# Kernel optimization log

Hardware: AMD Instinct MI355X
Metric: run time of the kernel (lower is better)

## Reference

```python
import jax, jax.numpy as jnp
import numpy as np

C_M, C_Z, H, C_HID = 256, 128, 8, 32
N_SEQ, N_RES = 64, 384
INF = 1e9
EPS = 1e-5


def layernorm(x, w, b):
    mu = jnp.mean(x, axis=-1, keepdims=True)
    var = jnp.mean(jnp.square(x - mu), axis=-1, keepdims=True)
    return (x - mu) * jax.lax.rsqrt(var + EPS) * w + b


def setup_inputs() -> dict:
    key = jax.random.key(0)
    ks = jax.random.split(key, 6)
    m = jax.random.normal(ks[0], (N_SEQ, N_RES, C_M), dtype=jnp.float32)
    z = jax.random.normal(ks[1], (N_RES, N_RES, C_Z), dtype=jnp.float32)
    mask = jnp.ones((N_SEQ, N_RES), dtype=jnp.float32)
    return {
        "m": m,
        "z": z,
        "mask": mask,
        "ln_m_w": jnp.ones((C_M,), jnp.float32),
        "ln_m_b": jnp.zeros((C_M,), jnp.float32),
        "ln_z_w": jnp.ones((C_Z,), jnp.float32),
        "ln_z_b": jnp.zeros((C_Z,), jnp.float32),
        "W_z": jax.random.normal(ks[2], (C_Z, H), jnp.float32) * 0.05,
        "W_v": jax.random.normal(ks[3], (C_M, H * C_HID), jnp.float32) * 0.05,
        "W_g": jax.random.normal(ks[4], (C_M, H * C_HID), jnp.float32) * 0.05,
        "W_o": jax.random.normal(ks[5], (H * C_HID, C_M), jnp.float32) * 0.05,
    }


def reference(m, z, mask, ln_m_w, ln_m_b, ln_z_w, ln_z_b, W_z, W_v, W_g, W_o):
    S, N = m.shape[0], m.shape[1]
    # mask: max over MSA rows, keepdim -> [1, N]; bias -> [1,1,1,N]
    mask_max = jnp.max(mask, axis=-2, keepdims=True)
    mask_bias = (INF * (mask_max - 1.0))[:, None, None, :]  # [1,1,1,N]
    # pair bias: LN(z) @ W_z -> [N,N,H] -> [H,N,N]
    zb = layernorm(z, ln_z_w, ln_z_b) @ W_z  # [N,N,H]
    zb = jnp.transpose(zb, (2, 0, 1))  # [H,N,N]
    # LN on m
    m_ln = layernorm(m, ln_m_w, ln_m_b)  # [S,N,C_m]
    # values: [S,N,H*c] -> [S,H,N,c]
    v = (m_ln @ W_v).reshape(S, N, H, C_HID).transpose(0, 2, 1, 3)
    # attention weights from summed biases (no QK): [1,H,N,N] after broadcast
    a = jax.nn.softmax(mask_bias + zb[None], axis=-1)  # [1,H,N,N]
    # o = a @ v  -> [S,H,N,c]
    o = jnp.einsum('hqk,shkc->shqc', a[0], v)
    o = o.transpose(0, 2, 1, 3)  # [S,N,H,c]
    # sigmoid gate
    g = jax.nn.sigmoid(m_ln @ W_g).reshape(S, N, H, C_HID)
    o = (o * g).reshape(S, N, H * C_HID)
    return o @ W_o  # [S,N,C_m]
```

## Files before the change

### kernel.cpp

```cpp
#include <hip/hip_runtime.h>
#include <math.h>

#define S 64
#define NRES 384
#define CM 256
#define CZ 128
#define NH 8
#define CH 32
#define HC 256
#define NROW 147456

typedef unsigned short u16;
typedef __attribute__((ext_vector_type(8))) short bf16x8;
typedef __attribute__((ext_vector_type(4))) float f32x4;
typedef __attribute__((ext_vector_type(8))) unsigned short ushort8;
typedef __attribute__((ext_vector_type(4))) unsigned short ushort4_t;

#define OFF_BIAS 0
#define OFF_WT   200704
#define OFF_WOT  462848
#define OFF_A    593920
#define OFF_VT   2953216
#define OFF_G    15536128
#define OFF_O    28119040
#define OFF_MLN  40701952
#define OFF_ZB   OFF_O

__device__ __forceinline__ u16 f2bf(float f) {
    union { float f; unsigned int u; } v; v.f = f;
    unsigned int u = v.u;
    u += 0x7fff + ((u >> 16) & 1);
    return (u16)(u >> 16);
}
__device__ __forceinline__ float bf2f(u16 b) {
    union { float f; unsigned int u; } v; v.u = ((unsigned int)b) << 16;
    return v.f;
}
__device__ __forceinline__ void gload16(const u16* g, u16* l) {
    __builtin_amdgcn_global_load_lds(
        (const __attribute__((address_space(1))) void*)g,
        (__attribute__((address_space(3))) void*)l, 16, 0, 0);
}

__global__ __launch_bounds__(256) void k_stage1(
        const float* __restrict__ z, const float* __restrict__ Wz,
        const float* __restrict__ lzw, const float* __restrict__ lzb,
        const float* __restrict__ mask,
        const float* __restrict__ Wv, const float* __restrict__ Wg,
        const float* __restrict__ Wo, const float* __restrict__ m,
        const float* __restrict__ lmw, const float* __restrict__ lmb,
        float* __restrict__ zb, float* __restrict__ bias,
        u16* __restrict__ Wt, u16* __restrict__ Wot, u16* __restrict__ mln) {
    const int bid = blockIdx.x, tid = threadIdx.x;
    if (bid < 1152) {
        __shared__ u16 sWWT[16 * 128];
        __shared__ float sPart[2][2][8];
        const int wave = tid >> 6, lane = tid & 63;
        const int rl = lane & 15, kg = lane >> 4;
        if (tid < 128) {
            const int c = tid;
            const float4 wz0 = *(const float4*)&Wz[c * 8];
            const float4 wz1 = *(const float4*)&Wz[c * 8 + 4];
            const float lw = lzw[c], lbv = lzb[c];
            float wzv[8] = {wz0.x, wz0.y, wz0.z, wz0.w, wz1.x, wz1.y, wz1.z, wz1.w};
            float ww[8], wb[8];
            #pragma unroll
            for (int h = 0; h < 8; ++h) {
                ww[h] = lw * wzv[h];
                wb[h] = lbv * wzv[h];
                sWWT[h * 128 + c] = f2bf(ww[h]);
                sWWT[(8 + h) * 128 + c] = 0;
            }
            #pragma unroll
            for (int h = 0; h < 8; ++h) {
                #pragma unroll
                for (int off = 1; off < 64; off <<= 1) {
                    ww[h] += __shfl_xor(ww[h], off);
                    wb[h] += __shfl_xor(wb[h], off);
                }
            }
            if (lane == 0) {
                #pragma unroll
                for (int h = 0; h < 8; ++h) {
                    sPart[wave][0][h] = ww[h];
                    sPart[wave][1][h] = wb[h];
                }
            }
        }
        __syncthreads();
        const float c1 = (rl < 8) ? (sPart[0][0][rl] + sPart[1][0][rl]) : 0.f;
        const float c2 = (rl < 8) ? (sPart[0][1][rl] + sPart[1][1][rl]) : 0.f;
        bf16x8 bfr[4];
        #pragma unroll
        for (int t = 0; t < 4; ++t)
            bfr[t] = *(const bf16x8*)&sWWT[rl * 128 + kg * 8 + t * 32];
        #pragma unroll
        for (int it = 0; it < 2; ++it) {
            const int row0 = bid * 128 + it * 64 + wave * 16;
            const float* zrow = z + (size_t)(row0 + rl) * CZ + kg * 8;
            bf16x8 af[4];
            float sm = 0.f, sq = 0.f;
            #pragma unroll
            for (int t = 0; t < 4; ++t) {
                const float4 x0 = *(const float4*)&zrow[t * 32];
                const float4 x1 = *(const float4*)&zrow[t * 32 + 4];
                float xs[8] = {x0.x, x0.y, x0.z, x0.w, x1.x, x1.y, x1.z, x1.w};
                u16 tmp[8];
                #pragma unroll
                for (int e = 0; e < 8; ++e) {
                    sm += xs[e]; sq += xs[e] * xs[e];
                    tmp[e] = f2bf(xs[e]);
                }
                af[t] = *(bf16x8*)tmp;
            }
            sm += __shfl_xor(sm, 16); sq += __shfl_xor(sq, 16);
            sm += __shfl_xor(sm, 32); sq += __shfl_xor(sq, 32);
            const float mu = sm * (1.0f / CZ);
            const float var = sq * (1.0f / CZ) - mu * mu;
            const float rs = rsqrtf(var + 1e-5f);
            f32x4 acc = {};
            #pragma unroll
            for (int t = 0; t < 4; ++t)
                acc = __builtin_amdgcn_mfma_f32_16x16x32_bf16(af[t], bfr[t], acc, 0, 0, 0);
            f32x4 pv;
            #pragma unroll
            for (int r = 0; r < 4; ++r) {
                const int rr = kg * 4 + r;
                const float mu_r = __shfl(mu, rr);
                const float rs_r = __shfl(rs, rr);
                pv[r] = rs_r * (acc[r] - mu_r * c1) + c2;
            }
            if (rl < 8)
                *(f32x4*)&zb[(size_t)rl * NROW + row0 + kg * 4] = pv;
        }
    } else if (bid < 1154) {
        const int k = (bid - 1152) * 256 + tid;
        if (k < NRES) {
            float mx = -1e30f;
            for (int s = 0; s < S; ++s) mx = fmaxf(mx, mask[s * NRES + k]);
            bias[k] = 1e9f * (mx - 1.0f);
        }
    } else if (bid < 1666) {
        const int i = (bid - 1154) * 256 + tid;
        const int n = i >> 8, k = i & 255;
        const float v = (n < HC) ? Wv[(size_t)k * HC + n] : Wg[(size_t)k * HC + (n - HC)];
        Wt[i] = f2bf(v);
    } else if (bid < 1922) {
        const int i = (bid - 1666) * 256 + tid;
        const int n = i >> 8, k = i & 255;
        Wot[i] = f2bf(Wo[(size_t)k * CM + n]);
    } else {
        const int row = (bid - 1922) * 4 + (tid >> 6);
        const int lane = tid & 63;
        const float4 x = *(const float4*)&m[(size_t)row * CM + lane * 4];
        float sm = x.x + x.y + x.z + x.w;
        float sq = x.x*x.x + x.y*x.y + x.z*x.z + x.w*x.w;
        #pragma unroll
        for (int off = 32; off >= 1; off >>= 1) {
            sm += __shfl_xor(sm, off);
            sq += __shfl_xor(sq, off);
        }
        const float mu = sm * (1.0f / CM);
        const float var = sq * (1.0f / CM) - mu * mu;
        const float rs = rsqrtf(var + 1e-5f);
        const float4 w4 = *(const float4*)&lmw[lane * 4];
        const float4 b4 = *(const float4*)&lmb[lane * 4];
        u16 t4[4];
        t4[0] = f2bf((x.x - mu) * rs * w4.x + b4.x);
        t4[1] = f2bf((x.y - mu) * rs * w4.y + b4.y);
        t4[2] = f2bf((x.z - mu) * rs * w4.z + b4.z);
        t4[3] = f2bf((x.w - mu) * rs * w4.w + b4.w);
        *(ushort4_t*)&mln[(size_t)row * CM + lane * 4] = *(ushort4_t*)t4;
    }
}

__global__ __launch_bounds__(256) void k_stage2(
        const u16* __restrict__ mln, const u16* __restrict__ Wt,
        const float* __restrict__ zb, const float* __restrict__ bias,
        u16* __restrict__ vt, u16* __restrict__ g_, u16* __restrict__ a_out) {
    __shared__ u16 As[128][32];
    __shared__ u16 Bs[128][32];
    const int bid = blockIdx.x, tid = threadIdx.x;
    if (bid >= 768) {
        const int w = (bid - 768) * 4 + (tid >> 6);
        const int lane = tid & 63;
        const int h = w & 7, q = w >> 3;
        const float* zbh = zb + (size_t)h * NROW + (size_t)q * NRES;
        float v[6];
        float mx = -1e30f;
        #pragma unroll
        for (int t = 0; t < 6; ++t) {
            const int k = lane + 64 * t;
            v[t] = zbh[k] + bias[k];
            mx = fmaxf(mx, v[t]);
        }
        #pragma unroll
        for (int off = 32; off >= 1; off >>= 1) mx = fmaxf(mx, __shfl_xor(mx, off));
        float sum = 0.f;
        #pragma unroll
        for (int t = 0; t < 6; ++t) { v[t] = expf(v[t] - mx); sum += v[t]; }
        #pragma unroll
        for (int off = 32; off >= 1; off >>= 1) sum += __shfl_xor(sum, off);
        const float inv = 1.0f / sum;
        #pragma unroll
        for (int t = 0; t < 6; ++t)
            a_out[((size_t)h * NRES + q) * NRES + lane + 64 * t] = f2bf(v[t] * inv);
        return;
    }
    const int xcd = bid & 7, idx = bid >> 3;
    const int nt = idx & 3, mt = xcd * 24 + (idx >> 2);
    const int m0 = mt * 128, n0 = nt * 128;
    const int wave = tid >> 6, lane = tid & 63;
    const int wm = (wave >> 1) * 64, wn = (wave & 1) * 64;
    const int rl = lane & 15, kg = lane >> 4;
    const int lr = lane >> 2, lk = (lane & 3) * 8;
    const int wr = wave * 32;
    const u16* ag  = mln + (size_t)(m0 + wr + lr) * CM + lk;
    const u16* ag2 = ag + 16 * CM;
    const u16* bg  = Wt + (size_t)(n0 + wr + lr) * CM + lk;
    const u16* bg2 = bg + 16 * CM;
    u16* al  = &As[wr][0];
    u16* al2 = &As[wr + 16][0];
    u16* bl  = &Bs[wr][0];
    u16* bl2 = &Bs[wr + 16][0];
    const bool vhalf = (n0 < HC);
    f32x4 acc[4][4] = {};
    for (int kt = 0; kt < CM; kt += 32) {
        if (kt) __syncthreads();
        gload16(ag + kt, al);  gload16(ag2 + kt, al2);
        gload16(bg + kt, bl);  gload16(bg2 + kt, bl2);
        __syncthreads();
        bf16x8 af[4], bfr[4];
        #pragma unroll
        for (int i = 0; i < 4; ++i) af[i]  = *(const bf16x8*)&As[wm + i*16 + rl][kg*8];
        #pragma unroll
        for (int j = 0; j < 4; ++j) bfr[j] = *(const bf16x8*)&Bs[wn + j*16 + rl][kg*8];
        if (vhalf) {
            #pragma unroll
            for (int j = 0; j < 4; ++j)
                #pragma unroll
                for (int i = 0; i < 4; ++i)
                    acc[j][i] = __builtin_amdgcn_mfma_f32_16x16x32_bf16(bfr[j], af[i], acc[j][i], 0, 0, 0);
        } else {
            #pragma unroll
            for (int i = 0; i < 4; ++i)
                #pragma unroll
                for (int j = 0; j < 4; ++j)
                    acc[i][j] = __builtin_amdgcn_mfma_f32_16x16x32_bf16(af[i], bfr[j], acc[i][j], 0, 0, 0);
        }
    }
    if (vhalf) {
        #pragma unroll
        for (int j = 0; j < 4; ++j)
            #pragma unroll
            for (int r = 0; r < 4; ++r) {
                const int vcol = n0 + wn + j*16 + kg*4 + r;
                const int h = vcol >> 5, c = vcol & 31;
                #pragma unroll
                for (int i = 0; i < 4; ++i) {
                    const int mrowb = m0 + wm + i*16;
                    const int s = mrowb / NRES;
                    const int nn = mrowb - s * NRES + rl;
                    vt[(((size_t)h * S + s) * CH + c) * NRES + nn] = f2bf(acc[j][i][r]);
                }
            }
    } else {
        #pragma unroll
        for (int i = 0; i < 4; ++i)
            #pragma unroll
            for (int r = 0; r < 4; ++r) {
                const int row = m0 + wm + i*16 + kg*4 + r;
                #pragma unroll
                for (int j = 0; j < 4; ++j) {
                    const int gc = n0 + wn + j*16 + rl - HC;
                    g_[(size_t)row * HC + gc] = f2bf(1.0f / (1.0f + expf(-acc[i][j][r])));
                }
            }
    }
}

__global__ __launch_bounds__(256) void k_attn2(const u16* __restrict__ a_,
        const u16* __restrict__ vt, u16* __restrict__ o_) {
    __shared__ u16 As[128][32];
    __shared__ u16 Bs[128][32];
    const int tid = threadIdx.x;
    const int h = blockIdx.x & 7, rem = blockIdx.x >> 3;
    const int mt = rem >> 4, nt = rem & 15;
    const int q0 = mt * 128, sc0 = nt * 128;
    const int wave = tid >> 6, lane = tid & 63;
    const int wm = (wave >> 1) * 64, wn = (wave & 1) * 64;
    const int rl = lane & 15, kg = lane >> 4;
    const int lr = lane >> 2, lk = (lane & 3) * 8;
    const int wr = wave * 32;
    const u16* ag  = a_ + (size_t)h * NRES * NRES + (size_t)(q0 + wr + lr) * NRES + lk;
    const u16* ag2 = ag + 16 * NRES;
    const u16* bg  = vt + (size_t)h * S * CH * NRES + (size_t)(sc0 + wr + lr) * NRES + lk;
    const u16* bg2 = bg + 16 * NRES;
    u16* al  = &As[wr][0];
    u16* al2 = &As[wr + 16][0];
    u16* bl  = &Bs[wr][0];
    u16* bl2 = &Bs[wr + 16][0];
    f32x4 acc[4][4] = {};
    for (int kt = 0; kt < NRES; kt += 32) {
        if (kt) __syncthreads();
        gload16(ag + kt, al);  gload16(ag2 + kt, al2);
        gload16(bg + kt, bl);  gload16(bg2 + kt, bl2);
        __syncthreads();
        bf16x8 af[4], bfr[4];
        #pragma unroll
        for (int i = 0; i < 4; ++i) af[i]  = *(const bf16x8*)&As[wm + i*16 + rl][kg*8];
        #pragma unroll
        for (int j = 0; j < 4; ++j) bfr[j] = *(const bf16x8*)&Bs[wn + j*16 + rl][kg*8];
        #pragma unroll
        for (int i = 0; i < 4; ++i)
            #pragma unroll
            for (int j = 0; j < 4; ++j)
                acc[i][j] = __builtin_amdgcn_mfma_f32_16x16x32_bf16(af[i], bfr[j], acc[i][j], 0, 0, 0);
    }
    #pragma unroll
    for (int i = 0; i < 4; ++i)
        #pragma unroll
        for (int r = 0; r < 4; ++r) {
            const int q = q0 + wm + i*16 + kg*4 + r;
            #pragma unroll
            for (int j = 0; j < 4; ++j) {
                const int sc = sc0 + wn + j*16 + rl;
                const int s = sc >> 5, c = sc & 31;
                o_[(((size_t)s * NRES + q) * NH + h) * CH + c] = f2bf(acc[i][j][r]);
            }
        }
}

__global__ __launch_bounds__(256) void k_gemm_out(const u16* __restrict__ o_,
        const u16* __restrict__ g_, const u16* __restrict__ Wot,
        float* __restrict__ out) {
    __shared__ u16 As[128][40];
    __shared__ u16 Bs[128][32];
    const int tid = threadIdx.x;
    const int xcd = blockIdx.x & 7, idx = blockIdx.x >> 3;
    const int nt = idx & 1, mt = xcd * 24 + (idx >> 1);
    const int m0 = mt * 128, n0 = nt * 128;
    const int wave = tid >> 6, lane = tid & 63;
    const int wm = (wave >> 1) * 64, wn = (wave & 1) * 64;
    const int rl = lane & 15, kg = lane >> 4;
    const int lr = lane >> 2, lk = (lane & 3) * 8;
    const int wr = wave * 32;
    const int sr = tid >> 1, sh = (tid & 1) * 16;
    const u16* orow = o_ + (size_t)(m0 + sr) * HC;
    const u16* grow = g_ + (size_t)(m0 + sr) * HC;
    const u16* bg  = Wot + (size_t)(n0 + wr + lr) * HC + lk;
    const u16* bg2 = bg + 16 * HC;
    u16* bl  = &Bs[wr][0];
    u16* bl2 = &Bs[wr + 16][0];
    f32x4 acc[4][4] = {};
    for (int kt = 0; kt < HC; kt += 32) {
        if (kt) __syncthreads();
        gload16(bg + kt, bl);  gload16(bg2 + kt, bl2);
        {
            u16 tmp[16];
            const ushort8 ov0 = *(const ushort8*)&orow[kt + sh];
            const ushort8 ov1 = *(const ushort8*)&orow[kt + sh + 8];
            const ushort8 gv0 = *(const ushort8*)&grow[kt + sh];
            const ushort8 gv1 = *(const ushort8*)&grow[kt + sh + 8];
            #pragma unroll
            for (int p = 0; p < 8; ++p) {
                tmp[p]     = f2bf(bf2f(ov0[p]) * bf2f(gv0[p]));
                tmp[p + 8] = f2bf(bf2f(ov1[p]) * bf2f(gv1[p]));
            }
            *(ushort8*)&As[sr][sh]     = *(ushort8*)&tmp[0];
            *(ushort8*)&As[sr][sh + 8] = *(ushort8*)&tmp[8];
        }
        __syncthreads();
        bf16x8 af[4], bfr[4];
        #pragma unroll
        for (int i = 0; i < 4; ++i) af[i]  = *(const bf16x8*)&As[wm + i*16 + rl][kg*8];
        #pragma unroll
        for (int j = 0; j < 4; ++j) bfr[j] = *(const bf16x8*)&Bs[wn + j*16 + rl][kg*8];
        #pragma unroll
        for (int i = 0; i < 4; ++i)
            #pragma unroll
            for (int j = 0; j < 4; ++j)
                acc[i][j] = __builtin_amdgcn_mfma_f32_16x16x32_bf16(af[i], bfr[j], acc[i][j], 0, 0, 0);
    }
    #pragma unroll
    for (int i = 0; i < 4; ++i)
        #pragma unroll
        for (int r = 0; r < 4; ++r) {
            const int row = m0 + wm + i*16 + kg*4 + r;
            #pragma unroll
            for (int j = 0; j < 4; ++j)
                out[(size_t)row * CM + n0 + wn + j*16 + rl] = acc[i][j][r];
        }
}

extern "C" void kernel_launch(void* const* d_in, const int* in_sizes, int n_in,
                              void* d_out, int out_size, void* d_ws, size_t ws_size,
                              hipStream_t stream) {
    const float* m      = (const float*)d_in[0];
    const float* z      = (const float*)d_in[1];
    const float* mask   = (const float*)d_in[2];
    const float* ln_m_w = (const float*)d_in[3];
    const float* ln_m_b = (const float*)d_in[4];
    const float* ln_z_w = (const float*)d_in[5];
    const float* ln_z_b = (const float*)d_in[6];
    const float* Wz     = (const float*)d_in[7];
    const float* Wv     = (const float*)d_in[8];
    const float* Wg     = (const float*)d_in[9];
    const float* Wo     = (const float*)d_in[10];
    float* out = (float*)d_out;
    char* ws = (char*)d_ws;

    float* bias = (float*)(ws + OFF_BIAS);
    u16* Wt     = (u16*)(ws + OFF_WT);
    u16* Wot    = (u16*)(ws + OFF_WOT);
    u16* a      = (u16*)(ws + OFF_A);
    u16* vtw    = (u16*)(ws + OFF_VT);
    u16* gw     = (u16*)(ws + OFF_G);
    u16* ow     = (u16*)(ws + OFF_O);
    u16* mlnw   = (u16*)(ws + OFF_MLN);
    float* zbw  = (float*)(ws + OFF_ZB);

    k_stage1<<<8066, 256, 0, stream>>>(z, Wz, ln_z_w, ln_z_b, mask, Wv, Wg, Wo,
                                       m, ln_m_w, ln_m_b, zbw, bias, Wt, Wot, mlnw);
    k_stage2<<<1536, 256, 0, stream>>>(mlnw, Wt, zbw, bias, vtw, gw, a);
    k_attn2<<<384, 256, 0, stream>>>(a, vtw, ow);
    k_gemm_out<<<384, 256, 0, stream>>>(ow, gw, Wot, out);
}
```

Before: 76.77 us.

## Fuse pair-bias LayerNorm projection with softmax per query row in shared memory

Moves the LN(z)@W_z computation out of stage1 and into the softmax blocks of the main kernel. Each of 384 blocks now handles one query row: it stages z through shared memory, computes all 8 head logits with MFMA into LDS, then runs the softmax directly. This removes the fp32 zb round-trip through global memory and one dependency boundary. In exchange, z is processed by only 384 blocks using about 50KB of shared memory each, which may lower occupancy and parallelism for the z-read phase.

```diff
diff --git a/kernel.cpp b/kernel.cpp
--- a/kernel.cpp
+++ b/kernel.cpp
@@ -24,7 +24,6 @@
 #define OFF_G    15536128
 #define OFF_O    28119040
 #define OFF_MLN  40701952
-#define OFF_ZB   OFF_O
 
 __device__ __forceinline__ u16 f2bf(float f) {
     union { float f; unsigned int u; } v; v.f = f;
@@ -42,115 +41,32 @@
         (__attribute__((address_space(3))) void*)l, 16, 0, 0);
 }
 
-__global__ __launch_bounds__(256) void k_stage1(
-        const float* __restrict__ z, const float* __restrict__ Wz,
-        const float* __restrict__ lzw, const float* __restrict__ lzb,
+__global__ __launch_bounds__(256) void k_misc(
         const float* __restrict__ mask,
         const float* __restrict__ Wv, const float* __restrict__ Wg,
         const float* __restrict__ Wo, const float* __restrict__ m,
         const float* __restrict__ lmw, const float* __restrict__ lmb,
-        float* __restrict__ zb, float* __restrict__ bias,
-        u16* __restrict__ Wt, u16* __restrict__ Wot, u16* __restrict__ mln) {
+        float* __restrict__ bias, u16* __restrict__ Wt, u16* __restrict__ Wot,
+        u16* __restrict__ mln) {
     const int bid = blockIdx.x, tid = threadIdx.x;
-    if (bid < 1152) {
-        __shared__ u16 sWWT[16 * 128];
-        __shared__ float sPart[2][2][8];
-        const int wave = tid >> 6, lane = tid & 63;
-        const int rl = lane & 15, kg = lane >> 4;
-        if (tid < 128) {
-            const int c = tid;
-            const float4 wz0 = *(const float4*)&Wz[c * 8];
-            const float4 wz1 = *(const float4*)&Wz[c * 8 + 4];
-            const float lw = lzw[c], lbv = lzb[c];
-            float wzv[8] = {wz0.x, wz0.y, wz0.z, wz0.w, wz1.x, wz1.y, wz1.z, wz1.w};
-            float ww[8], wb[8];
-            #pragma unroll
-            for (int h = 0; h < 8; ++h) {
-                ww[h] = lw * wzv[h];
-                wb[h] = lbv * wzv[h];
-                sWWT[h * 128 + c] = f2bf(ww[h]);
-                sWWT[(8 + h) * 128 + c] = 0;
-            }
-            #pragma unroll
-            for (int h = 0; h < 8; ++h) {
-                #pragma unroll
-                for (int off = 1; off < 64; off <<= 1) {
-                    ww[h] += __shfl_xor(ww[h], off);
-                    wb[h] += __shfl_xor(wb[h], off);
-                }
-            }
-            if (lane == 0) {
-                #pragma unroll
-                for (int h = 0; h < 8; ++h) {
-                    sPart[wave][0][h] = ww[h];
-                    sPart[wave][1][h] = wb[h];
-                }
-            }
-        }
-        __syncthreads();
-        const float c1 = (rl < 8) ? (sPart[0][0][rl] + sPart[1][0][rl]) : 0.f;
-        const float c2 = (rl < 8) ? (sPart[0][1][rl] + sPart[1][1][rl]) : 0.f;
-        bf16x8 bfr[4];
-        #pragma unroll
-        for (int t = 0; t < 4; ++t)
-            bfr[t] = *(const bf16x8*)&sWWT[rl * 128 + kg * 8 + t * 32];
-        #pragma unroll
-        for (int it = 0; it < 2; ++it) {
-            const int row0 = bid * 128 + it * 64 + wave * 16;
-            const float* zrow = z + (size_t)(row0 + rl) * CZ + kg * 8;
-            bf16x8 af[4];
-            float sm = 0.f, sq = 0.f;
-            #pragma unroll
-            for (int t = 0; t < 4; ++t) {
-                const float4 x0 = *(const float4*)&zrow[t * 32];
-                const float4 x1 = *(const float4*)&zrow[t * 32 + 4];
-                float xs[8] = {x0.x, x0.y, x0.z, x0.w, x1.x, x1.y, x1.z, x1.w};
-                u16 tmp[8];
-                #pragma unroll
-                for (int e = 0; e < 8; ++e) {
-                    sm += xs[e]; sq += xs[e] * xs[e];
-                    tmp[e] = f2bf(xs[e]);
-                }
-                af[t] = *(bf16x8*)tmp;
-            }
-            sm += __shfl_xor(sm, 16); sq += __shfl_xor(sq, 16);
-            sm += __shfl_xor(sm, 32); sq += __shfl_xor(sq, 32);
-            const float mu = sm * (1.0f / CZ);
-            const float var = sq * (1.0f / CZ) - mu * mu;
-            const float rs = rsqrtf(var + 1e-5f);
-            f32x4 acc = {};
-            #pragma unroll
-            for (int t = 0; t < 4; ++t)
-                acc = __builtin_amdgcn_mfma_f32_16x16x32_bf16(af[t], bfr[t], acc, 0, 0, 0);
-            f32x4 pv;
-            #pragma unroll
-            for (int r = 0; r < 4; ++r) {
-                const int rr = kg * 4 + r;
-                const float mu_r = __shfl(mu, rr);
-                const float rs_r = __shfl(rs, rr);
-                pv[r] = rs_r * (acc[r] - mu_r * c1) + c2;
-            }
-            if (rl < 8)
-                *(f32x4*)&zb[(size_t)rl * NROW + row0 + kg * 4] = pv;
-        }
-    } else if (bid < 1154) {
-        const int k = (bid - 1152) * 256 + tid;
+    if (bid < 2) {
+        const int k = bid * 256 + tid;
         if (k < NRES) {
             float mx = -1e30f;
             for (int s = 0; s < S; ++s) mx = fmaxf(mx, mask[s * NRES + k]);
             bias[k] = 1e9f * (mx - 1.0f);
         }
-    } else if (bid < 1666) {
-        const int i = (bid - 1154) * 256 + tid;
+    } else if (bid < 514) {
+        const int i = (bid - 2) * 256 + tid;
         const int n = i >> 8, k = i & 255;
         const float v = (n < HC) ? Wv[(size_t)k * HC + n] : Wg[(size_t)k * HC + (n - HC)];
         Wt[i] = f2bf(v);
-    } else if (bid < 1922) {
-        const int i = (bid - 1666) * 256 + tid;
+    } else if (bid < 770) {
+        const int i = (bid - 514) * 256 + tid;
         const int n = i >> 8, k = i & 255;
         Wot[i] = f2bf(Wo[(size_t)k * CM + n]);
     } else {
-        const int row = (bid - 1922) * 4 + (tid >> 6);
+        const int row = (bid - 770) * 4 + (tid >> 6);
         const int lane = tid & 63;
         const float4 x = *(const float4*)&m[(size_t)row * CM + lane * 4];
         float sm = x.x + x.y + x.z + x.w;
@@ -174,55 +90,151 @@
     }
 }
 
-__global__ __launch_bounds__(256) void k_stage2(
+__global__ __launch_bounds__(256) void k_main(
+        const float* __restrict__ z, const float* __restrict__ Wz,
+        const float* __restrict__ lzw, const float* __restrict__ lzb,
+        const float* __restrict__ bias,
         const u16* __restrict__ mln, const u16* __restrict__ Wt,
-        const float* __restrict__ zb, const float* __restrict__ bias,
-        u16* __restrict__ vt, u16* __restrict__ g_, u16* __restrict__ a_out) {
-    __shared__ u16 As[128][32];
-    __shared__ u16 Bs[128][32];
+        u16* __restrict__ a_out, u16* __restrict__ vt, u16* __restrict__ g_) {
+    __shared__ float smem[12544];
     const int bid = blockIdx.x, tid = threadIdx.x;
-    if (bid >= 768) {
-        const int w = (bid - 768) * 4 + (tid >> 6);
-        const int lane = tid & 63;
-        const int h = w & 7, q = w >> 3;
-        const float* zbh = zb + (size_t)h * NROW + (size_t)q * NRES;
-        float v[6];
-        float mx = -1e30f;
-        #pragma unroll
-        for (int t = 0; t < 6; ++t) {
-            const int k = lane + 64 * t;
-            v[t] = zbh[k] + bias[k];
-            mx = fmaxf(mx, v[t]);
-        }
-        #pragma unroll
-        for (int off = 32; off >= 1; off >>= 1) mx = fmaxf(mx, __shfl_xor(mx, off));
-        float sum = 0.f;
-        #pragma unroll
-        for (int t = 0; t < 6; ++t) { v[t] = expf(v[t] - mx); sum += v[t]; }
-        #pragma unroll
-        for (int off = 32; off >= 1; off >>= 1) sum += __shfl_xor(sum, off);
-        const float inv = 1.0f / sum;
-        #pragma unroll
-        for (int t = 0; t < 6; ++t)
-            a_out[((size_t)h * NRES + q) * NRES + lane + 64 * t] = f2bf(v[t] * inv);
+    const int wave = tid >> 6, lane = tid & 63;
+    const int rl = lane & 15, kg = lane >> 4;
+
+    if (bid < 384) {
+        const int q = bid;
+        float* sZ   = smem;
+        float* sLg  = smem + 8320;
+        u16*  sW    = (u16*)(smem + 11456);
+        float* sPart = smem + 12480;
+
+        if (tid < 128) {
+            const int c = tid;
+            const float4 wz0 = *(const float4*)&Wz[c * 8];
+            const float4 wz1 = *(const float4*)&Wz[c * 8 + 4];
+            const float lw = lzw[c], lbv = lzb[c];
+            float wzv[8] = {wz0.x, wz0.y, wz0.z, wz0.w, wz1.x, wz1.y, wz1.z, wz1.w};
+            float ww[8], wb[8];
+            #pragma unroll
+            for (int h = 0; h < 8; ++h) {
+                ww[h] = lw * wzv[h];
+                wb[h] = lbv * wzv[h];
+                sW[h * 128 + c] = f2bf(ww[h]);
+                sW[(8 + h) * 128 + c] = 0;
+            }
+            #pragma unroll
+            for (int h = 0; h < 8; ++h) {
+                #pragma unroll
+                for (int off = 1; off < 64; off <<= 1) {
+                    ww[h] += __shfl_xor(ww[h], off);
+                    wb[h] += __shfl_xor(wb[h], off);
+                }
+            }
+            if (lane == 0) {
+                #pragma unroll
+                for (int h = 0; h < 8; ++h) {
+                    sPart[wave * 16 + h]     = ww[h];
+                    sPart[wave * 16 + 8 + h] = wb[h];
+                }
+            }
+        }
+        __syncthreads();
+        const float c1 = (rl < 8) ? (sPart[rl] + sPart[16 + rl]) : 0.f;
+        const float c2 = (rl < 8) ? (sPart[8 + rl] + sPart[24 + rl]) : 0.f;
+        bf16x8 bfr[4];
+        #pragma unroll
+        for (int t = 0; t < 4; ++t)
+            bfr[t] = *(const bf16x8*)&sW[rl * 128 + kg * 8 + t * 32];
+
+        float* sZw = sZ + wave * 2080;
+        const float4* zq = (const float4*)(z + (size_t)q * NRES * CZ);
+        for (int c = 0; c < 6; ++c) {
+            const float4* src = zq + (size_t)(c * 64 + wave * 16) * (CZ / 4);
+            #pragma unroll
+            for (int p = 0; p < 8; ++p) {
+                const int fi = p * 64 + lane;
+                const int r = fi >> 5, c4 = fi & 31;
+                *(float4*)&sZw[r * 130 + c4 * 4] = src[fi];
+            }
+            float sm = 0.f, sq = 0.f;
+            bf16x8 af[4];
+            #pragma unroll
+            for (int t = 0; t < 4; ++t) {
+                const f32x4 x0 = *(const f32x4*)&sZw[rl * 130 + t * 32 + kg * 8];
+                const f32x4 x1 = *(const f32x4*)&sZw[rl * 130 + t * 32 + kg * 8 + 4];
+                float xs[8] = {x0[0], x0[1], x0[2], x0[3], x1[0], x1[1], x1[2], x1[3]};
+                u16 tmp[8];
+                #pragma unroll
+                for (int e = 0; e < 8; ++e) {
+                    sm += xs[e]; sq += xs[e] * xs[e];
+                    tmp[e] = f2bf(xs[e]);
+                }
+                af[t] = *(bf16x8*)tmp;
+            }
+            sm += __shfl_xor(sm, 16); sq += __shfl_xor(sq, 16);
+            sm += __shfl_xor(sm, 32); sq += __shfl_xor(sq, 32);
+            const float mu = sm * (1.0f / CZ);
+            const float var = sq * (1.0f / CZ) - mu * mu;
+            const float rs = rsqrtf(var + 1e-5f);
+            f32x4 acc = {};
+            #pragma unroll
+            for (int t = 0; t < 4; ++t)
+                acc = __builtin_amdgcn_mfma_f32_16x16x32_bf16(af[t], bfr[t], acc, 0, 0, 0);
+            f32x4 pv;
+            #pragma unroll
+            for (int r = 0; r < 4; ++r) {
+                const int rr = kg * 4 + r;
+                const float mu_r = __shfl(mu, rr);
+                const float rs_r = __shfl(rs, rr);
+                pv[r] = rs_r * (acc[r] - mu_r * c1) + c2;
+            }
+            if (rl < 8)
+                *(f32x4*)&sLg[rl * 392 + c * 64 + wave * 16 + kg * 4] = pv;
+        }
+        __syncthreads();
+        #pragma unroll
+        for (int hh = 0; hh < 2; ++hh) {
+            const int h = wave + hh * 4;
+            float v[6];
+            float mx = -1e30f;
+            #pragma unroll
+            for (int t = 0; t < 6; ++t) {
+                const int k = lane + 64 * t;
+                v[t] = sLg[h * 392 + k] + bias[k];
+                mx = fmaxf(mx, v[t]);
+            }
+            #pragma unroll
+            for (int off = 32; off >= 1; off >>= 1) mx = fmaxf(mx, __shfl_xor(mx, off));
+            float sum = 0.f;
+            #pragma unroll
+            for (int t = 0; t < 6; ++t) { v[t] = expf(v[t] - mx); sum += v[t]; }
+            #pragma unroll
+            for (int off = 32; off >= 1; off >>= 1) sum += __shfl_xor(sum, off);
+            const float inv = 1.0f / sum;
+            #pragma unroll
+            for (int t = 0; t < 6; ++t)
+                a_out[((size_t)h * NRES + q) * NRES + lane + 64 * t] = f2bf(v[t] * inv);
+        }
         return;
     }
-    const int xcd = bid & 7, idx = bid >> 3;
+
+    const int bb = bid - 384;
+    const int xcd = bb & 7, idx = bb >> 3;
     const int nt = idx & 3, mt = xcd * 24 + (idx >> 2);
     const int m0 = mt * 128, n0 = nt * 128;
-    const int wave = tid >> 6, lane = tid & 63;
     const int wm = (wave >> 1) * 64, wn = (wave & 1) * 64;
-    const int rl = lane & 15, kg = lane >> 4;
     const int lr = lane >> 2, lk = (lane & 3) * 8;
     const int wr = wave * 32;
+    u16* As = (u16*)smem;
+    u16* Bs = As + 128 * 32;
     const u16* ag  = mln + (size_t)(m0 + wr + lr) * CM + lk;
     const u16* ag2 = ag + 16 * CM;
     const u16* bg  = Wt + (size_t)(n0 + wr + lr) * CM + lk;
     const u16* bg2 = bg + 16 * CM;
-    u16* al  = &As[wr][0];
-    u16* al2 = &As[wr + 16][0];
-    u16* bl  = &Bs[wr][0];
-    u16* bl2 = &Bs[wr + 16][0];
+    u16* al  = As + wr * 32;
+    u16* al2 = As + (wr + 16) * 32;
+    u16* bl  = Bs + wr * 32;
+    u16* bl2 = Bs + (wr + 16) * 32;
     const bool vhalf = (n0 < HC);
     f32x4 acc[4][4] = {};
     for (int kt = 0; kt < CM; kt += 32) {
@@ -232,9 +244,9 @@
         __syncthreads();
         bf16x8 af[4], bfr[4];
         #pragma unroll
-        for (int i = 0; i < 4; ++i) af[i]  = *(const bf16x8*)&As[wm + i*16 + rl][kg*8];
-        #pragma unroll
-        for (int j = 0; j < 4; ++j) bfr[j] = *(const bf16x8*)&Bs[wn + j*16 + rl][kg*8];
+        for (int i = 0; i < 4; ++i) af[i]  = *(const bf16x8*)&As[(wm + i*16 + rl) * 32 + kg*8];
+        #pragma unroll
+        for (int j = 0; j < 4; ++j) bfr[j] = *(const bf16x8*)&Bs[(wn + j*16 + rl) * 32 + kg*8];
         if (vhalf) {
             #pragma unroll
             for (int j = 0; j < 4; ++j)
@@ -418,11 +430,11 @@
     u16* gw     = (u16*)(ws + OFF_G);
     u16* ow     = (u16*)(ws + OFF_O);
     u16* mlnw   = (u16*)(ws + OFF_MLN);
-    float* zbw  = (float*)(ws + OFF_ZB);
-
-    k_stage1<<<8066, 256, 0, stream>>>(z, Wz, ln_z_w, ln_z_b, mask, Wv, Wg, Wo,
-                                       m, ln_m_w, ln_m_b, zbw, bias, Wt, Wot, mlnw);
-    k_stage2<<<1536, 256, 0, stream>>>(mlnw, Wt, zbw, bias, vtw, gw, a);
+
+    k_misc<<<6914, 256, 0, stream>>>(mask, Wv, Wg, Wo, m, ln_m_w, ln_m_b,
+                                     bias, Wt, Wot, mlnw);
+    k_main<<<1152, 256, 0, stream>>>(z, Wz, ln_z_w, ln_z_b, bias, mlnw, Wt,
+                                     a, vtw, gw);
     k_attn2<<<384, 256, 0, stream>>>(a, vtw, ow);
     k_gemm_out<<<384, 256, 0, stream>>>(ow, gw, Wot, out);
 }
```

After: 97.04 us. 1.26x slower.

## Stage z rows through LDS with coalesced loads and halve rows per block

Applied to the files above, without the earlier changes.

The z layernorm+projection part of stage1 now loads each block's 64 rows of z into padded shared memory using fully coalesced float4 loads, then reads fragments from LDS instead of strided global loads. Blocks process 64 rows instead of 128, doubling the block count for that branch, and grid offsets for the other branches are shifted to match. This targets poor global coalescing of the per-lane strided z reads. In exchange it adds about 37KB of static shared memory to every block of the fused kernel, including branches that never use it, which may reduce occupancy.

```diff
diff --git a/kernel.cpp b/kernel.cpp
--- a/kernel.cpp
+++ b/kernel.cpp
@@ -51,12 +51,15 @@
         const float* __restrict__ lmw, const float* __restrict__ lmb,
         float* __restrict__ zb, float* __restrict__ bias,
         u16* __restrict__ Wt, u16* __restrict__ Wot, u16* __restrict__ mln) {
+    __shared__ float smem[9376];
     const int bid = blockIdx.x, tid = threadIdx.x;
-    if (bid < 1152) {
-        __shared__ u16 sWWT[16 * 128];
-        __shared__ float sPart[2][2][8];
+    if (bid < 2304) {
+        float* sZ   = smem;
+        u16*  sW    = (u16*)(smem + 8320);
+        float* sPart = smem + 9344;
         const int wave = tid >> 6, lane = tid & 63;
         const int rl = lane & 15, kg = lane >> 4;
+        const int row0 = bid * 64;
         if (tid < 128) {
             const int c = tid;
             const float4 wz0 = *(const float4*)&Wz[c * 8];
@@ -68,8 +71,8 @@
             for (int h = 0; h < 8; ++h) {
                 ww[h] = lw * wzv[h];
                 wb[h] = lbv * wzv[h];
-                sWWT[h * 128 + c] = f2bf(ww[h]);
-                sWWT[(8 + h) * 128 + c] = 0;
+                sW[h * 128 + c] = f2bf(ww[h]);
+                sW[(8 + h) * 128 + c] = 0;
             }
             #pragma unroll
             for (int h = 0; h < 8; ++h) {
@@ -82,75 +85,78 @@
             if (lane == 0) {
                 #pragma unroll
                 for (int h = 0; h < 8; ++h) {
-                    sPart[wave][0][h] = ww[h];
-                    sPart[wave][1][h] = wb[h];
+                    sPart[wave * 16 + h]     = ww[h];
+                    sPart[wave * 16 + 8 + h] = wb[h];
                 }
             }
         }
+        const float4* zq = (const float4*)(z + (size_t)row0 * CZ);
+        #pragma unroll
+        for (int i = 0; i < 8; ++i) {
+            const int fi = tid + i * 256;
+            const int r = fi >> 5, c4 = fi & 31;
+            *(float4*)&sZ[r * 130 + c4 * 4] = zq[fi];
+        }
         __syncthreads();
-        const float c1 = (rl < 8) ? (sPart[0][0][rl] + sPart[1][0][rl]) : 0.f;
-        const float c2 = (rl < 8) ? (sPart[0][1][rl] + sPart[1][1][rl]) : 0.f;
+        const float c1 = (rl < 8) ? (sPart[rl] + sPart[16 + rl]) : 0.f;
+        const float c2 = (rl < 8) ? (sPart[8 + rl] + sPart[24 + rl]) : 0.f;
         bf16x8 bfr[4];
         #pragma unroll
         for (int t = 0; t < 4; ++t)
-            bfr[t] = *(const bf16x8*)&sWWT[rl * 128 + kg * 8 + t * 32];
-        #pragma unroll
-        for (int it = 0; it < 2; ++it) {
-            const int row0 = bid * 128 + it * 64 + wave * 16;
-            const float* zrow = z + (size_t)(row0 + rl) * CZ + kg * 8;
-            bf16x8 af[4];
-            float sm = 0.f, sq = 0.f;
-            #pragma unroll
-            for (int t = 0; t < 4; ++t) {
-                const float4 x0 = *(const float4*)&zrow[t * 32];
-                const float4 x1 = *(const float4*)&zrow[t * 32 + 4];
-                float xs[8] = {x0.x, x0.y, x0.z, x0.w, x1.x, x1.y, x1.z, x1.w};
-                u16 tmp[8];
-                #pragma unroll
-                for (int e = 0; e < 8; ++e) {
-                    sm += xs[e]; sq += xs[e] * xs[e];
-                    tmp[e] = f2bf(xs[e]);
-                }
-                af[t] = *(bf16x8*)tmp;
-            }
-            sm += __shfl_xor(sm, 16); sq += __shfl_xor(sq, 16);
-            sm += __shfl_xor(sm, 32); sq += __shfl_xor(sq, 32);
-            const float mu = sm * (1.0f / CZ);
-            const float var = sq * (1.0f / CZ) - mu * mu;
-            const float rs = rsqrtf(var + 1e-5f);
-            f32x4 acc = {};
-            #pragma unroll
-            for (int t = 0; t < 4; ++t)
-                acc = __builtin_amdgcn_mfma_f32_16x16x32_bf16(af[t], bfr[t], acc, 0, 0, 0);
-            f32x4 pv;
-            #pragma unroll
-            for (int r = 0; r < 4; ++r) {
-                const int rr = kg * 4 + r;
-                const float mu_r = __shfl(mu, rr);
-                const float rs_r = __shfl(rs, rr);
-                pv[r] = rs_r * (acc[r] - mu_r * c1) + c2;
-            }
-            if (rl < 8)
-                *(f32x4*)&zb[(size_t)rl * NROW + row0 + kg * 4] = pv;
-        }
-    } else if (bid < 1154) {
-        const int k = (bid - 1152) * 256 + tid;
+            bfr[t] = *(const bf16x8*)&sW[rl * 128 + kg * 8 + t * 32];
+        const float* zrow = sZ + (wave * 16 + rl) * 130 + kg * 8;
+        bf16x8 af[4];
+        float sm = 0.f, sq = 0.f;
+        #pragma unroll
+        for (int t = 0; t < 4; ++t) {
+            const f32x4 x0 = *(const f32x4*)&zrow[t * 32];
+            const f32x4 x1 = *(const f32x4*)&zrow[t * 32 + 4];
+            float xs[8] = {x0[0], x0[1], x0[2], x0[3], x1[0], x1[1], x1[2], x1[3]};
+            u16 tmp[8];
+            #pragma unroll
+            for (int e = 0; e < 8; ++e) {
+                sm += xs[e]; sq += xs[e] * xs[e];
+                tmp[e] = f2bf(xs[e]);
+            }
+            af[t] = *(bf16x8*)tmp;
+        }
+        sm += __shfl_xor(sm, 16); sq += __shfl_xor(sq, 16);
+        sm += __shfl_xor(sm, 32); sq += __shfl_xor(sq, 32);
+        const float mu = sm * (1.0f / CZ);
+        const float var = sq * (1.0f / CZ) - mu * mu;
+        const float rs = rsqrtf(var + 1e-5f);
+        f32x4 acc = {};
+        #pragma unroll
+        for (int t = 0; t < 4; ++t)
+            acc = __builtin_amdgcn_mfma_f32_16x16x32_bf16(af[t], bfr[t], acc, 0, 0, 0);
+        f32x4 pv;
+        #pragma unroll
+        for (int r = 0; r < 4; ++r) {
+            const int rr = kg * 4 + r;
+            const float mu_r = __shfl(mu, rr);
+            const float rs_r = __shfl(rs, rr);
+            pv[r] = rs_r * (acc[r] - mu_r * c1) + c2;
+        }
+        if (rl < 8)
+            *(f32x4*)&zb[(size_t)rl * NROW + row0 + wave * 16 + kg * 4] = pv;
+    } else if (bid < 2306) {
+        const int k = (bid - 2304) * 256 + tid;
         if (k < NRES) {
             float mx = -1e30f;
             for (int s = 0; s < S; ++s) mx = fmaxf(mx, mask[s * NRES + k]);
             bias[k] = 1e9f * (mx - 1.0f);
         }
-    } else if (bid < 1666) {
-        const int i = (bid - 1154) * 256 + tid;
+    } else if (bid < 2818) {
+        const int i = (bid - 2306) * 256 + tid;
         const int n = i >> 8, k = i & 255;
         const float v = (n < HC) ? Wv[(size_t)k * HC + n] : Wg[(size_t)k * HC + (n - HC)];
         Wt[i] = f2bf(v);
-    } else if (bid < 1922) {
-        const int i = (bid - 1666) * 256 + tid;
+    } else if (bid < 3074) {
+        const int i = (bid - 2818) * 256 + tid;
         const int n = i >> 8, k = i & 255;
         Wot[i] = f2bf(Wo[(size_t)k * CM + n]);
     } else {
-        const int row = (bid - 1922) * 4 + (tid >> 6);
+        const int row = (bid - 3074) * 4 + (tid >> 6);
         const int lane = tid & 63;
         const float4 x = *(const float4*)&m[(size_t)row * CM + lane * 4];
         float sm = x.x + x.y + x.z + x.w;
@@ -420,7 +426,7 @@
     u16* mlnw   = (u16*)(ws + OFF_MLN);
     float* zbw  = (float*)(ws + OFF_ZB);
 
-    k_stage1<<<8066, 256, 0, stream>>>(z, Wz, ln_z_w, ln_z_b, mask, Wv, Wg, Wo,
+    k_stage1<<<9218, 256, 0, stream>>>(z, Wz, ln_z_w, ln_z_b, mask, Wv, Wg, Wo,
                                        m, ln_m_w, ln_m_b, zbw, bias, Wt, Wot, mlnw);
     k_stage2<<<1536, 256, 0, stream>>>(mlnw, Wt, zbw, bias, vtw, gw, a);
     k_attn2<<<384, 256, 0, stream>>>(a, vtw, ow);
```

Result: slower. 83.60 us (+8.9%).

## Split pair-bias LN+projection into dedicated kernel with coalesced LDS-staged z loads

Applied to the files above, without the earlier changes.

Moves the folded LayerNorm weight and bias sums (WWT, C1, C2) into a small precompute block of a separate misc kernel, so they are no longer recomputed in every pair-bias block. A new k_zb kernel reads z fully coalesced, converts it to bf16 and stages it through swizzled LDS before the MFMA projection. Each block now loops over 4 row groups. This targets the strided z loads and the redundant per-block weight prep. In exchange it adds an extra kernel launch and a global round trip for the weights.

```diff
diff --git a/kernel.cpp b/kernel.cpp
--- a/kernel.cpp
+++ b/kernel.cpp
@@ -17,6 +17,9 @@
 typedef __attribute__((ext_vector_type(4))) unsigned short ushort4_t;
 
 #define OFF_BIAS 0
+#define OFF_WWT  8192
+#define OFF_C1   16384
+#define OFF_C2   16448
 #define OFF_WT   200704
 #define OFF_WOT  462848
 #define OFF_A    593920
@@ -42,21 +45,26 @@
         (__attribute__((address_space(3))) void*)l, 16, 0, 0);
 }
 
-__global__ __launch_bounds__(256) void k_stage1(
-        const float* __restrict__ z, const float* __restrict__ Wz,
+__global__ __launch_bounds__(256) void k_misc(
+        const float* __restrict__ mask, const float* __restrict__ Wz,
         const float* __restrict__ lzw, const float* __restrict__ lzb,
-        const float* __restrict__ mask,
         const float* __restrict__ Wv, const float* __restrict__ Wg,
         const float* __restrict__ Wo, const float* __restrict__ m,
         const float* __restrict__ lmw, const float* __restrict__ lmb,
-        float* __restrict__ zb, float* __restrict__ bias,
+        float* __restrict__ bias, u16* __restrict__ WWT,
+        float* __restrict__ C1, float* __restrict__ C2,
         u16* __restrict__ Wt, u16* __restrict__ Wot, u16* __restrict__ mln) {
+    __shared__ float sP[2][2][8];
     const int bid = blockIdx.x, tid = threadIdx.x;
-    if (bid < 1152) {
-        __shared__ u16 sWWT[16 * 128];
-        __shared__ float sPart[2][2][8];
+    if (bid < 2) {
+        const int k = bid * 256 + tid;
+        if (k < NRES) {
+            float mx = -1e30f;
+            for (int s = 0; s < S; ++s) mx = fmaxf(mx, mask[s * NRES + k]);
+            bias[k] = 1e9f * (mx - 1.0f);
+        }
+    } else if (bid == 2) {
         const int wave = tid >> 6, lane = tid & 63;
-        const int rl = lane & 15, kg = lane >> 4;
         if (tid < 128) {
             const int c = tid;
             const float4 wz0 = *(const float4*)&Wz[c * 8];
@@ -68,8 +76,8 @@
             for (int h = 0; h < 8; ++h) {
                 ww[h] = lw * wzv[h];
                 wb[h] = lbv * wzv[h];
-                sWWT[h * 128 + c] = f2bf(ww[h]);
-                sWWT[(8 + h) * 128 + c] = 0;
+                WWT[h * 128 + c] = f2bf(ww[h]);
+                WWT[(8 + h) * 128 + c] = 0;
             }
             #pragma unroll
             for (int h = 0; h < 8; ++h) {
@@ -82,75 +90,27 @@
             if (lane == 0) {
                 #pragma unroll
                 for (int h = 0; h < 8; ++h) {
-                    sPart[wave][0][h] = ww[h];
-                    sPart[wave][1][h] = wb[h];
+                    sP[wave][0][h] = ww[h];
+                    sP[wave][1][h] = wb[h];
                 }
             }
         }
         __syncthreads();
-        const float c1 = (rl < 8) ? (sPart[0][0][rl] + sPart[1][0][rl]) : 0.f;
-        const float c2 = (rl < 8) ? (sPart[0][1][rl] + sPart[1][1][rl]) : 0.f;
-        bf16x8 bfr[4];
-        #pragma unroll
-        for (int t = 0; t < 4; ++t)
-            bfr[t] = *(const bf16x8*)&sWWT[rl * 128 + kg * 8 + t * 32];
-        #pragma unroll
-        for (int it = 0; it < 2; ++it) {
-            const int row0 = bid * 128 + it * 64 + wave * 16;
-            const float* zrow = z + (size_t)(row0 + rl) * CZ + kg * 8;
-            bf16x8 af[4];
-            float sm = 0.f, sq = 0.f;
-            #pragma unroll
-            for (int t = 0; t < 4; ++t) {
-                const float4 x0 = *(const float4*)&zrow[t * 32];
-                const float4 x1 = *(const float4*)&zrow[t * 32 + 4];
-                float xs[8] = {x0.x, x0.y, x0.z, x0.w, x1.x, x1.y, x1.z, x1.w};
-                u16 tmp[8];
-                #pragma unroll
-                for (int e = 0; e < 8; ++e) {
-                    sm += xs[e]; sq += xs[e] * xs[e];
-                    tmp[e] = f2bf(xs[e]);
-                }
-                af[t] = *(bf16x8*)tmp;
-            }
-            sm += __shfl_xor(sm, 16); sq += __shfl_xor(sq, 16);
-            sm += __shfl_xor(sm, 32); sq += __shfl_xor(sq, 32);
-            const float mu = sm * (1.0f / CZ);
-            const float var = sq * (1.0f / CZ) - mu * mu;
-            const float rs = rsqrtf(var + 1e-5f);
-            f32x4 acc = {};
-            #pragma unroll
-            for (int t = 0; t < 4; ++t)
-                acc = __builtin_amdgcn_mfma_f32_16x16x32_bf16(af[t], bfr[t], acc, 0, 0, 0);
-            f32x4 pv;
-            #pragma unroll
-            for (int r = 0; r < 4; ++r) {
-                const int rr = kg * 4 + r;
-                const float mu_r = __shfl(mu, rr);
-                const float rs_r = __shfl(rs, rr);
-                pv[r] = rs_r * (acc[r] - mu_r * c1) + c2;
-            }
-            if (rl < 8)
-                *(f32x4*)&zb[(size_t)rl * NROW + row0 + kg * 4] = pv;
-        }
-    } else if (bid < 1154) {
-        const int k = (bid - 1152) * 256 + tid;
-        if (k < NRES) {
-            float mx = -1e30f;
-            for (int s = 0; s < S; ++s) mx = fmaxf(mx, mask[s * NRES + k]);
-            bias[k] = 1e9f * (mx - 1.0f);
-        }
-    } else if (bid < 1666) {
-        const int i = (bid - 1154) * 256 + tid;
+        if (tid < 8) {
+            C1[tid] = sP[0][0][tid] + sP[1][0][tid];
+            C2[tid] = sP[0][1][tid] + sP[1][1][tid];
+        }
+    } else if (bid < 515) {
+        const int i = (bid - 3) * 256 + tid;
         const int n = i >> 8, k = i & 255;
         const float v = (n < HC) ? Wv[(size_t)k * HC + n] : Wg[(size_t)k * HC + (n - HC)];
         Wt[i] = f2bf(v);
-    } else if (bid < 1922) {
-        const int i = (bid - 1666) * 256 + tid;
+    } else if (bid < 771) {
+        const int i = (bid - 515) * 256 + tid;
         const int n = i >> 8, k = i & 255;
         Wot[i] = f2bf(Wo[(size_t)k * CM + n]);
     } else {
-        const int row = (bid - 1922) * 4 + (tid >> 6);
+        const int row = (bid - 771) * 4 + (tid >> 6);
         const int lane = tid & 63;
         const float4 x = *(const float4*)&m[(size_t)row * CM + lane * 4];
         float sm = x.x + x.y + x.z + x.w;
@@ -171,6 +131,81 @@
         t4[2] = f2bf((x.z - mu) * rs * w4.z + b4.z);
         t4[3] = f2bf((x.w - mu) * rs * w4.w + b4.w);
         *(ushort4_t*)&mln[(size_t)row * CM + lane * 4] = *(ushort4_t*)t4;
+    }
+}
+
+__global__ __launch_bounds__(256) void k_zb(
+        const float* __restrict__ z, const u16* __restrict__ WWT,
+        const float* __restrict__ C1, const float* __restrict__ C2,
+        float* __restrict__ zb) {
+    __shared__ u16 sZ[4][2048];
+    __shared__ float sSt[4][2][16];
+    const int tid = threadIdx.x, wave = tid >> 6, lane = tid & 63;
+    const int rl = lane & 15, kg = lane >> 4;
+    u16* myZ = &sZ[wave][0];
+    bf16x8 bfr[4];
+    #pragma unroll
+    for (int t = 0; t < 4; ++t)
+        bfr[t] = *(const bf16x8*)&WWT[rl * 128 + t * 32 + kg * 8];
+    const float c1 = (rl < 8) ? C1[rl] : 0.f;
+    const float c2 = (rl < 8) ? C2[rl] : 0.f;
+
+    #pragma unroll 1
+    for (int it = 0; it < 4; ++it) {
+        const int row0 = (blockIdx.x * 4 + it) * 64 + wave * 16;
+        const float4* zbase = (const float4*)(z + (size_t)row0 * CZ);
+        float smj[4], sqj[4];
+        #pragma unroll
+        for (int j = 0; j < 4; ++j) {
+            const int ci = lane + 64 * j;
+            const int rloc = ci >> 4, ch = ci & 15;
+            const float4 x0 = zbase[ci * 2];
+            const float4 x1 = zbase[ci * 2 + 1];
+            float xs[8] = {x0.x, x0.y, x0.z, x0.w, x1.x, x1.y, x1.z, x1.w};
+            float sm = 0.f, sq = 0.f;
+            u16 t8[8];
+            #pragma unroll
+            for (int e = 0; e < 8; ++e) {
+                sm += xs[e]; sq += xs[e] * xs[e];
+                t8[e] = f2bf(xs[e]);
+            }
+            smj[j] = sm; sqj[j] = sq;
+            *(ushort8*)&myZ[rloc * 128 + (ch ^ (rloc & 7)) * 8] = *(ushort8*)t8;
+        }
+        #pragma unroll
+        for (int j = 0; j < 4; ++j) {
+            #pragma unroll
+            for (int off = 1; off < 16; off <<= 1) {
+                smj[j] += __shfl_xor(smj[j], off);
+                sqj[j] += __shfl_xor(sqj[j], off);
+            }
+        }
+        if ((lane & 15) == 0) {
+            #pragma unroll
+            for (int j = 0; j < 4; ++j) {
+                const int r = (lane >> 4) + 4 * j;
+                const float mu = smj[j] * (1.0f / CZ);
+                const float var = sqj[j] * (1.0f / CZ) - mu * mu;
+                sSt[wave][0][r] = mu;
+                sSt[wave][1][r] = rsqrtf(var + 1e-5f);
+            }
+        }
+        bf16x8 af[4];
+        #pragma unroll
+        for (int t = 0; t < 4; ++t)
+            af[t] = *(const bf16x8*)&myZ[rl * 128 + ((t * 4 + kg) ^ (rl & 7)) * 8];
+        f32x4 acc = {};
+        #pragma unroll
+        for (int t = 0; t < 4; ++t)
+            acc = __builtin_amdgcn_mfma_f32_16x16x32_bf16(af[t], bfr[t], acc, 0, 0, 0);
+        f32x4 pv;
+        #pragma unroll
+        for (int r = 0; r < 4; ++r) {
+            const int rr = kg * 4 + r;
+            pv[r] = sSt[wave][1][rr] * (acc[r] - sSt[wave][0][rr] * c1) + c2;
+        }
+        if (rl < 8)
+            *(f32x4*)&zb[(size_t)rl * NROW + row0 + kg * 4] = pv;
     }
 }
 
@@ -411,6 +446,9 @@
     char* ws = (char*)d_ws;
 
     float* bias = (float*)(ws + OFF_BIAS);
+    u16* WWT    = (u16*)(ws + OFF_WWT);
+    float* C1   = (float*)(ws + OFF_C1);
+    float* C2   = (float*)(ws + OFF_C2);
     u16* Wt     = (u16*)(ws + OFF_WT);
     u16* Wot    = (u16*)(ws + OFF_WOT);
     u16* a      = (u16*)(ws + OFF_A);
@@ -420,8 +458,9 @@
     u16* mlnw   = (u16*)(ws + OFF_MLN);
     float* zbw  = (float*)(ws + OFF_ZB);
 
-    k_stage1<<<8066, 256, 0, stream>>>(z, Wz, ln_z_w, ln_z_b, mask, Wv, Wg, Wo,
-                                       m, ln_m_w, ln_m_b, zbw, bias, Wt, Wot, mlnw);
+    k_misc<<<6915, 256, 0, stream>>>(mask, Wz, ln_z_w, ln_z_b, Wv, Wg, Wo, m,
+                                     ln_m_w, ln_m_b, bias, WWT, C1, C2, Wt, Wot, mlnw);
+    k_zb<<<576, 256, 0, stream>>>(z, WWT, C1, C2, zbw);
     k_stage2<<<1536, 256, 0, stream>>>(mlnw, Wt, zbw, bias, vtw, gw, a);
     k_attn2<<<384, 256, 0, stream>>>(a, vtw, ow);
     k_gemm_out<<<384, 256, 0, stream>>>(ow, gw, Wot, out);
```

Result: slower. 85.45 us (+11.3%).
